# Kernel tuning notes

Hardware: AMD Instinct MI355X
Metric: run time of the kernel (lower is better)

Reference implementation:

```python
import jax, jax.numpy as jnp
import numpy as np

HIDDEN = 1152
NUM_HEADS = 16
HEAD_DIM = HIDDEN // NUM_HEADS  # 72
SEQ = 4096


def rotate_half(x):
    x1 = x[..., : x.shape[-1] // 2]
    x2 = x[..., x.shape[-1] // 2 :]
    return jnp.concatenate((-x2, x1), axis=-1)


def setup_inputs() -> dict:
    key = jax.random.key(0)
    ks = jax.random.split(key, 8)
    hidden_states = jax.random.normal(ks[0], (SEQ, HIDDEN), dtype=jnp.float32)
    cu_seqlens = jnp.sort(jax.random.randint(ks[1], (3,), 0, SEQ)).astype(jnp.int32)
    # rotary embeddings: realistic cos/sin tables
    pos = jnp.arange(SEQ, dtype=jnp.float32)[:, None]
    inv_freq = 1.0 / (10000.0 ** (jnp.arange(0, HEAD_DIM, 2, dtype=jnp.float32) / HEAD_DIM))
    freqs = pos * inv_freq[None, :]  # (SEQ, HEAD_DIM//2)
    emb = jnp.concatenate([freqs, freqs], axis=-1)  # (SEQ, HEAD_DIM)
    cos = jnp.cos(emb)
    sin = jnp.sin(emb)
    std = 0.02
    Wqkv = jax.random.normal(ks[2], (HIDDEN, 3 * HIDDEN), dtype=jnp.float32) * std
    bqkv = jnp.zeros((3 * HIDDEN,), dtype=jnp.float32)
    Wproj = jax.random.normal(ks[3], (HIDDEN, HIDDEN), dtype=jnp.float32) * std
    bproj = jnp.zeros((HIDDEN,), dtype=jnp.float32)
    return {
        "hidden_states": hidden_states,
        "cu_seqlens": cu_seqlens,
        "cos": cos,
        "sin": sin,
        "Wqkv": Wqkv,
        "bqkv": bqkv,
        "Wproj": Wproj,
        "bproj": bproj,
    }


def reference(hidden_states, cu_seqlens, cos, sin, Wqkv, bqkv, Wproj, bproj):
    seq_len = hidden_states.shape[0]
    scale = HEAD_DIM ** -0.5
    qkv = hidden_states @ Wqkv + bqkv  # (S, 3*H)
    qkv = qkv.reshape(seq_len, 3, NUM_HEADS, HEAD_DIM).transpose(1, 0, 2, 3)
    q, k, v = qkv[0], qkv[1], qkv[2]  # each (S, nH, hd)
    # inline RoPE in fp32
    orig_dtype = q.dtype
    qf = q.astype(jnp.float32)
    kf = k.astype(jnp.float32)
    c = cos[:, None, :].astype(jnp.float32)
    s = sin[:, None, :].astype(jnp.float32)
    q = (qf * c + rotate_half(qf) * s).astype(orig_dtype)
    k = (kf * c + rotate_half(kf) * s).astype(orig_dtype)
    # (nH, S, hd)
    q = q.transpose(1, 0, 2)
    k = k.transpose(1, 0, 2)
    v = v.transpose(1, 0, 2)
    attn = jnp.einsum('hqd,hkd->hqk', q, k) * scale
    attn = jax.nn.softmax(attn, axis=-1)
    out = jnp.einsum('hqk,hkd->hqd', attn, v)  # (nH, S, hd)
    out = out.transpose(1, 0, 2).reshape(seq_len, HIDDEN)
    return out @ Wproj + bproj
```

## Files before the change

### kernel.cpp

```cpp
#include <hip/hip_runtime.h>
#include <hip/hip_bf16.h>
#include <stdint.h>

#define SEQ 4096
#define HID 1152
#define NH  16
#define HD  72
#define N3  3456
#define DQ  80
#define QBLK 256
#define TILE_ELEMS 14336

typedef __bf16 bf16;
typedef __bf16 bf16x8 __attribute__((ext_vector_type(8)));
typedef float  f32x4  __attribute__((ext_vector_type(4)));
typedef float  f32x16 __attribute__((ext_vector_type(16)));
typedef uint32_t u32x4 __attribute__((ext_vector_type(4)));

#define EXP2F(x) __builtin_amdgcn_exp2f(x)
#define PLSWAP(a, b) asm("v_permlane32_swap_b32 %0, %1" : "+v"(a), "+v"(b))

__device__ __forceinline__ void gload_lds16(const void* g, void* l) {
    __builtin_amdgcn_global_load_lds(
        (__attribute__((address_space(1))) void*)(void*)g,
        (__attribute__((address_space(3))) void*)l, 16, 0, 0);
}
__device__ __forceinline__ uint16_t bfbits(float x) {
    return __builtin_bit_cast(uint16_t, (bf16)x);
}

__device__ __forceinline__ int xcd_swz(int orig, int nwg) {
    return (orig & 7) * (nwg >> 3) + (orig >> 3);
}

__global__ __launch_bounds__(256)
void prep(const float* __restrict__ hidden, const float* __restrict__ Wqkv,
          const float* __restrict__ Wproj, bf16* __restrict__ hid_b,
          bf16* __restrict__ WqkvT, bf16* __restrict__ WprojT)
{
    __shared__ float tl[32][33];
    int b = blockIdx.x, tid = threadIdx.x;
    if (b < 2304) {
        int i = b * 256 + tid;
        const float4* p = (const float4*)hidden + (size_t)i * 2;
        float4 a = p[0], c = p[1];
        bf16x8 o;
        o[0]=(bf16)a.x; o[1]=(bf16)a.y; o[2]=(bf16)a.z; o[3]=(bf16)a.w;
        o[4]=(bf16)c.x; o[5]=(bf16)c.y; o[6]=(bf16)c.z; o[7]=(bf16)c.w;
        ((bf16x8*)hid_b)[i] = o;
        return;
    }
    const float* in; bf16* out; int R, C, c0, r0;
    if (b < 6192) {
        int bb = b - 2304;
        in = Wqkv; out = WqkvT; R = HID; C = N3;
        c0 = (bb % 108) * 32; r0 = (bb / 108) * 32;
    } else {
        int bb = b - 6192;
        in = Wproj; out = WprojT; R = HID; C = HID;
        c0 = (bb % 36) * 32; r0 = (bb / 36) * 32;
    }
    int tx = tid & 31, ty = tid >> 5;
#pragma unroll
    for (int i = 0; i < 4; ++i)
        tl[ty + 8*i][tx] = in[(size_t)(r0 + ty + 8*i) * C + c0 + tx];
    __syncthreads();
#pragma unroll
    for (int i = 0; i < 4; ++i)
        out[(size_t)(c0 + ty + 8*i) * R + r0 + tx] = (bf16)tl[tx][ty + 8*i];
}

template<int OUT_F32>
__global__ __launch_bounds__(256)
void gemm_bt(const bf16* __restrict__ A, const bf16* __restrict__ BT,
             const float* __restrict__ bias, void* __restrict__ out,
             int M, int N, int K)
{
    __shared__ __align__(16) bf16 As[128 * 32];
    __shared__ __align__(16) bf16 Bs[128 * 32];
    int tid = threadIdx.x;
    int lane = tid & 63, w = tid >> 6;
    int wm = w & 1, wn = w >> 1;
    int nwg  = gridDim.x * gridDim.y;
    int wgid = xcd_swz(blockIdx.y * gridDim.x + blockIdx.x, nwg);
    int m0 = (wgid % gridDim.x) * 128, n0 = (wgid / gridDim.x) * 128;
    int lq = lane & 15, lk = lane >> 4;

    f32x4 acc[4][4] = {};

    for (int k0 = 0; k0 < K; k0 += 32) {
        __syncthreads();
#pragma unroll
        for (int i = 0; i < 2; ++i) {
            int c = w * 128 + i * 64 + lane;
            const bf16* ga = A  + (size_t)(m0 + (c >> 2)) * K + k0 + (c & 3) * 8;
            const bf16* gb = BT + (size_t)(n0 + (c >> 2)) * K + k0 + (c & 3) * 8;
            gload_lds16(ga, (char*)As + (w * 128 + i * 64) * 16);
            gload_lds16(gb, (char*)Bs + (w * 128 + i * 64) * 16);
        }
        __syncthreads();
        bf16x8 af[4], bfr[4];
#pragma unroll
        for (int m = 0; m < 4; ++m)
            af[m] = *(const bf16x8*)&As[(wm * 64 + m * 16 + lq) * 32 + lk * 8];
#pragma unroll
        for (int n = 0; n < 4; ++n)
            bfr[n] = *(const bf16x8*)&Bs[(wn * 64 + n * 16 + lq) * 32 + lk * 8];
#pragma unroll
        for (int m = 0; m < 4; ++m)
#pragma unroll
            for (int n = 0; n < 4; ++n)
                acc[m][n] = __builtin_amdgcn_mfma_f32_16x16x32_bf16(af[m], bfr[n], acc[m][n], 0, 0, 0);
    }

    int rb = m0 + wm * 64, cb = n0 + wn * 64;
#pragma unroll
    for (int m = 0; m < 4; ++m) {
#pragma unroll
        for (int n = 0; n < 4; ++n) {
            int col = cb + n * 16 + lq;
            float b = bias[col];
#pragma unroll
            for (int r = 0; r < 4; ++r) {
                int row = rb + m * 16 + lk * 4 + r;
                float v = acc[m][n][r] + b;
                if (OUT_F32) ((float*)out)[(size_t)row * N + col] = v;
                else         ((bf16*)out)[(size_t)row * N + col] = (bf16)v;
            }
        }
    }
}

__global__ __launch_bounds__(256)
void pack(const bf16* __restrict__ qkv, const float* __restrict__ cs,
          const float* __restrict__ sn, bf16* __restrict__ Qp,
          bf16* __restrict__ KVp)
{
    __shared__ __align__(16) bf16 tl[64][80];
    int b = blockIdx.x, tid = threadIdx.x;
    if (b < 32768) {
        int idx = b * 256 + tid;
        int dd = idx & 127;
        int s  = (idx >> 7) & (SEQ - 1);
        int h  = idx >> 19;
        float qv = 0.f, kv = 0.f;
        if (dd < HD) {
            const bf16* row = qkv + (size_t)s * N3 + h * HD;
            float c  = cs[s * HD + dd], si = sn[s * HD + dd];
            int   dp = (dd < 36) ? dd + 36 : dd - 36;
            float sg = (dd < 36) ? -1.f : 1.f;
            float qa = (float)row[dd],       qb = (float)row[dp];
            float ka = (float)row[HID + dd], kb = (float)row[HID + dp];
            qv = (qa * c + sg * qb * si) * (0.11785113019775793f * 1.4426950408889634f);
            kv =  ka * c + sg * kb * si;
        }
        int t = s >> 6, key = s & 63;
        int chunk = key * 16 + ((dd >> 3) ^ (key & 15));
        KVp[((size_t)(h * 64 + t)) * TILE_ELEMS + chunk * 8 + (dd & 7)] = (bf16)kv;
        if (dd < DQ) Qp[((size_t)h * SEQ + s) * DQ + dd] = (bf16)qv;
        return;
    }
    int bb = b - 32768;
    int t = bb & 63, h = bb >> 6, s0 = t * 64;
    for (int i = tid; i < 64 * 9; i += 256) {
        int key = i / 9, c8 = (i % 9) * 8;
        *(bf16x8*)&tl[key][c8] =
            *(const bf16x8*)&qkv[(size_t)(s0 + key) * N3 + 2 * HID + h * HD + c8];
    }
    __syncthreads();
    bf16* dst = KVp + ((size_t)(h * 64 + t)) * TILE_ELEMS + 8192;
    for (int vcid = tid; vcid < 768; vcid += 256) {
        int d = vcid >> 3, cpos = vcid & 7;
        int kb8 = (cpos ^ (d & 7)) << 3;
        bf16x8 v;
#pragma unroll
        for (int j = 0; j < 8; ++j)
            v[j] = (d < HD) ? tl[kb8 + j][d] : ((d == HD) ? (bf16)1.f : (bf16)0.f);
        *(bf16x8*)&dst[vcid * 8] = v;
    }
}

__global__ __launch_bounds__(512, 2)
void attn_fwd9(const bf16* __restrict__ Qp, const bf16* __restrict__ KVp,
               bf16* __restrict__ Oout)
{
    __shared__ __align__(16) char smem[114688];

    const int wgid = xcd_swz(blockIdx.x, gridDim.x);
    const int h  = wgid >> 4;
    const int q0 = (wgid & 15) * QBLK;
    const int tid = threadIdx.x, lane = tid & 63, w = tid >> 6;
    const int ql = lane & 31, hi = lane >> 5;
    const int q  = q0 + w * 32 + ql;

    bf16x8 qf[5];
    const bf16* qbase = Qp + ((size_t)h * SEQ + q) * DQ + hi * 8;
#pragma unroll
    for (int ks = 0; ks < 5; ++ks) qf[ks] = *(const bf16x8*)(qbase + ks * 16);

    int aK[5], aV[4];
#pragma unroll
    for (int ks = 0; ks < 5; ++ks)
        aK[ks] = ql * 256 + (((ks * 2 + hi) ^ (ql & 15)) * 16);
#pragma unroll
    for (int u = 0; u < 4; ++u)
        aV[u] = 16384 + ql * 128 + (((u * 2 + hi) ^ (ql & 7)) * 16);

    f32x16 o[3] = {};

    const bf16* kvbase = KVp + (size_t)h * (64 * TILE_ELEMS) + (size_t)tid * 8;

#define STAGE(T, DB) do {                                                      \
        const bf16* s_ = kvbase + (size_t)(T) * TILE_ELEMS;                    \
        char* d_ = smem + (DB) + tid * 16;                                     \
        _Pragma("unroll")                                                      \
        for (int j_ = 0; j_ < 3; ++j_)                                         \
            gload_lds16(s_ + j_ * 4096, d_ + j_ * 8192);                       \
        if (tid < 256) gload_lds16(s_ + 12288, d_ + 24576);                    \
    } while (0)

    auto compute = [&](const char* buf) {
        f32x16 sa = {}, sb = {};
        __builtin_amdgcn_s_setprio(1);
#pragma unroll
        for (int ks = 0; ks < 5; ++ks) {
            bf16x8 kf = *(const bf16x8*)(buf + aK[ks]);
            sa = __builtin_amdgcn_mfma_f32_32x32x16_bf16(kf, qf[ks], sa, 0, 0, 0);
        }
#pragma unroll
        for (int ks = 0; ks < 5; ++ks) {
            bf16x8 kf = *(const bf16x8*)(buf + 8192 + aK[ks]);
            sb = __builtin_amdgcn_mfma_f32_32x32x16_bf16(kf, qf[ks], sb, 0, 0, 0);
        }
        __builtin_amdgcn_s_setprio(0);

        uint32_t wd[16];
#pragma unroll
        for (int i = 0; i < 8; ++i) {
            wd[i]   = (uint32_t)bfbits(EXP2F(sa[2*i])) | ((uint32_t)bfbits(EXP2F(sa[2*i+1])) << 16);
            wd[8+i] = (uint32_t)bfbits(EXP2F(sb[2*i])) | ((uint32_t)bfbits(EXP2F(sb[2*i+1])) << 16);
        }

        PLSWAP(wd[0], wd[2]);   PLSWAP(wd[1], wd[3]);
        PLSWAP(wd[4], wd[6]);   PLSWAP(wd[5], wd[7]);
        PLSWAP(wd[8], wd[10]);  PLSWAP(wd[9], wd[11]);
        PLSWAP(wd[12], wd[14]); PLSWAP(wd[13], wd[15]);
        u32x4 u0 = {wd[0],wd[1],wd[2],wd[3]},   u1 = {wd[4],wd[5],wd[6],wd[7]};
        u32x4 u2 = {wd[8],wd[9],wd[10],wd[11]}, u3 = {wd[12],wd[13],wd[14],wd[15]};
        bf16x8 pb[4] = { __builtin_bit_cast(bf16x8, u0), __builtin_bit_cast(bf16x8, u1),
                         __builtin_bit_cast(bf16x8, u2), __builtin_bit_cast(bf16x8, u3) };

        __builtin_amdgcn_s_setprio(1);
#pragma unroll
        for (int db = 0; db < 3; ++db)
#pragma unroll
            for (int u = 0; u < 4; ++u) {
                bf16x8 vf = *(const bf16x8*)(buf + db * 4096 + aV[u]);
                o[db] = __builtin_amdgcn_mfma_f32_32x32x16_bf16(vf, pb[u], o[db], 0, 0, 0);
            }
        __builtin_amdgcn_s_setprio(0);
    };

#define WAIT86 do {                                                            \
        if (w < 4) asm volatile("s_waitcnt vmcnt(8)" ::: "memory");            \
        else       asm volatile("s_waitcnt vmcnt(6)" ::: "memory");            \
    } while (0)

    STAGE(0, 0); STAGE(1, 28672); STAGE(2, 57344);

    for (int tt = 0; tt < 60; tt += 4) {
#pragma unroll
        for (int j = 0; j < 4; ++j) {
            WAIT86;
            __builtin_amdgcn_s_barrier();
            STAGE(tt + j + 3, ((j + 3) & 3) * 28672);
            __builtin_amdgcn_sched_barrier(0);
            compute(smem + j * 28672);
        }
    }
    WAIT86;
    __builtin_amdgcn_s_barrier();
    STAGE(63, 86016);
    __builtin_amdgcn_sched_barrier(0);
    compute(smem);
    WAIT86;
    __builtin_amdgcn_s_barrier();
    __builtin_amdgcn_sched_barrier(0);
    compute(smem + 28672);
    if (w < 4) asm volatile("s_waitcnt vmcnt(4)" ::: "memory");
    else       asm volatile("s_waitcnt vmcnt(3)" ::: "memory");
    __builtin_amdgcn_s_barrier();
    __builtin_amdgcn_sched_barrier(0);
    compute(smem + 57344);
    asm volatile("s_waitcnt vmcnt(0)" ::: "memory");
    __builtin_amdgcn_s_barrier();
    __builtin_amdgcn_sched_barrier(0);
    compute(smem + 86016);
#undef STAGE
#undef WAIT86

    __syncthreads();
    bf16* Os = (bf16*)smem;
    {
        float lv  = o[2][4];
        float lo_ = __shfl_xor(lv, 32);
        float invl = 1.0f / (hi ? lo_ : lv);
        int qloc = w * 32 + ql;
#pragma unroll
        for (int db = 0; db < 3; ++db)
#pragma unroll
            for (int r = 0; r < 16; ++r) {
                int dloc = (r & 3) + 8 * (r >> 2) + 4 * hi;
                int d = db * 32 + dloc;
                if (d < HD) Os[qloc * 82 + d] = (bf16)(o[db][r] * invl);
            }
    }
    __syncthreads();
    for (int i = tid; i < QBLK * 36; i += 512) {
        int row = i / 36, c = i % 36;
        uint32_t val = *(const uint32_t*)((const char*)Os + row * 164 + c * 4);
        *(uint32_t*)((char*)Oout + (size_t)(q0 + row) * 2304 + h * 144 + c * 4) = val;
    }
}

extern "C" void kernel_launch(void* const* d_in, const int* in_sizes, int n_in,
                              void* d_out, int out_size, void* d_ws, size_t ws_size,
                              hipStream_t stream)
{
    const float* hidden = (const float*)d_in[0];
    const float* cosT  = (const float*)d_in[2];
    const float* sinT  = (const float*)d_in[3];
    const float* Wqkv  = (const float*)d_in[4];
    const float* bqkv  = (const float*)d_in[5];
    const float* Wproj = (const float*)d_in[6];
    const float* bproj = (const float*)d_in[7];

    char* ws = (char*)d_ws;
    size_t off = 0;
    auto alloc = [&](size_t bytes) {
        char* p = ws + off;
        off += (bytes + 255) & ~(size_t)255;
        return p;
    };
    bf16* hid_b  = (bf16*)alloc((size_t)SEQ * HID * 2);
    bf16* WqkvT  = (bf16*)alloc((size_t)N3  * HID * 2);
    bf16* WprojT = (bf16*)alloc((size_t)HID * HID * 2);
    bf16* qkv_b  = (bf16*)alloc((size_t)SEQ * N3  * 2);
    bf16* Qp     = (bf16*)alloc((size_t)NH * SEQ * DQ * 2);
    bf16* KVp    = (bf16*)alloc((size_t)NH * 64 * TILE_ELEMS * 2);
    bf16* attno  = hid_b;

    prep<<<7488, 256, 0, stream>>>(hidden, Wqkv, Wproj, hid_b, WqkvT, WprojT);
    gemm_bt<0><<<dim3(SEQ / 128, N3 / 128), 256, 0, stream>>>(hid_b, WqkvT, bqkv, qkv_b,
                                                              SEQ, N3, HID);
    pack<<<33792, 256, 0, stream>>>(qkv_b, cosT, sinT, Qp, KVp);
    attn_fwd9<<<dim3(SEQ / QBLK * NH), 512, 0, stream>>>(Qp, KVp, attno);
    gemm_bt<1><<<dim3(SEQ / 128, HID / 128), 256, 0, stream>>>(attno, WprojT, bproj, d_out,
                                                               SEQ, HID, HID);
}
```

Measured before the change: 223.9 us.

## Split KV sequence across two wave groups in 1024-thread attention blocks

The attention kernel now launches 1024 threads per block. Two groups of 8 waves each process alternate KV tiles, staged in pairs and double-buffered, and their partial outputs are summed through LDS at the end. The four-deep pipeline with fine-grained vmcnt waits is replaced by a simpler two-buffer scheme that waits on vmcnt(0) every iteration. The goal is more waves per block to hide latency, at the cost of a full drain each iteration, a reduction step, and LDS use of 120KB, which limits occupancy to one block per CU.

```diff
diff --git a/kernel.cpp b/kernel.cpp
--- a/kernel.cpp
+++ b/kernel.cpp
@@ -180,18 +180,19 @@
     }
 }
 
-__global__ __launch_bounds__(512, 2)
-void attn_fwd9(const bf16* __restrict__ Qp, const bf16* __restrict__ KVp,
-               bf16* __restrict__ Oout)
-{
-    __shared__ __align__(16) char smem[114688];
+__global__ __launch_bounds__(1024, 4)
+void attn_fwd10(const bf16* __restrict__ Qp, const bf16* __restrict__ KVp,
+                bf16* __restrict__ Oout)
+{
+    __shared__ __align__(16) char smem[122880];
 
     const int wgid = xcd_swz(blockIdx.x, gridDim.x);
     const int h  = wgid >> 4;
     const int q0 = (wgid & 15) * QBLK;
     const int tid = threadIdx.x, lane = tid & 63, w = tid >> 6;
+    const int wg = w & 7, kh = w >> 3;
     const int ql = lane & 31, hi = lane >> 5;
-    const int q  = q0 + w * 32 + ql;
+    const int q  = q0 + wg * 32 + ql;
 
     bf16x8 qf[5];
     const bf16* qbase = Qp + ((size_t)h * SEQ + q) * DQ + hi * 8;
@@ -201,35 +202,43 @@
     int aK[5], aV[4];
 #pragma unroll
     for (int ks = 0; ks < 5; ++ks)
-        aK[ks] = ql * 256 + (((ks * 2 + hi) ^ (ql & 15)) * 16);
+        aK[ks] = kh * 28672 + ql * 256 + (((ks * 2 + hi) ^ (ql & 15)) * 16);
 #pragma unroll
     for (int u = 0; u < 4; ++u)
-        aV[u] = 16384 + ql * 128 + (((u * 2 + hi) ^ (ql & 7)) * 16);
+        aV[u] = kh * 28672 + 16384 + ql * 128 + (((u * 2 + hi) ^ (ql & 7)) * 16);
 
     f32x16 o[3] = {};
 
-    const bf16* kvbase = KVp + (size_t)h * (64 * TILE_ELEMS) + (size_t)tid * 8;
-
-#define STAGE(T, DB) do {                                                      \
-        const bf16* s_ = kvbase + (size_t)(T) * TILE_ELEMS;                    \
-        char* d_ = smem + (DB) + tid * 16;                                     \
+    const bf16* kvsrc = KVp + (size_t)h * (64 * TILE_ELEMS) + (size_t)tid * 8;
+
+#define STAGE(P, BASE) do {                                                    \
+        const bf16* s_ = kvsrc + (size_t)(P) * 28672;                          \
+        char* d_ = smem + (BASE) + tid * 16;                                   \
         _Pragma("unroll")                                                      \
         for (int j_ = 0; j_ < 3; ++j_)                                         \
-            gload_lds16(s_ + j_ * 4096, d_ + j_ * 8192);                       \
-        if (tid < 256) gload_lds16(s_ + 12288, d_ + 24576);                    \
+            gload_lds16(s_ + j_ * 8192, d_ + j_ * 16384);                      \
+        if (tid < 512) gload_lds16(s_ + 24576, d_ + 49152);                    \
     } while (0)
 
-    auto compute = [&](const char* buf) {
+    STAGE(0, 0);
+    int stageBase = 65536;
+    asm volatile("s_waitcnt vmcnt(0)" ::: "memory");
+    __builtin_amdgcn_s_barrier();
+
+    for (int t = 0; t < 32; ++t) {
+        __builtin_amdgcn_sched_barrier(0);
+        if (t + 1 < 32) STAGE(t + 1, stageBase);
+
         f32x16 sa = {}, sb = {};
         __builtin_amdgcn_s_setprio(1);
 #pragma unroll
         for (int ks = 0; ks < 5; ++ks) {
-            bf16x8 kf = *(const bf16x8*)(buf + aK[ks]);
+            bf16x8 kf = *(const bf16x8*)(smem + aK[ks]);
             sa = __builtin_amdgcn_mfma_f32_32x32x16_bf16(kf, qf[ks], sa, 0, 0, 0);
         }
 #pragma unroll
         for (int ks = 0; ks < 5; ++ks) {
-            bf16x8 kf = *(const bf16x8*)(buf + 8192 + aK[ks]);
+            bf16x8 kf = *(const bf16x8*)(smem + aK[ks] + 8192);
             sb = __builtin_amdgcn_mfma_f32_32x32x16_bf16(kf, qf[ks], sb, 0, 0, 0);
         }
         __builtin_amdgcn_s_setprio(0);
@@ -255,57 +264,48 @@
         for (int db = 0; db < 3; ++db)
 #pragma unroll
             for (int u = 0; u < 4; ++u) {
-                bf16x8 vf = *(const bf16x8*)(buf + db * 4096 + aV[u]);
+                bf16x8 vf = *(const bf16x8*)(smem + aV[u] + db * 4096);
                 o[db] = __builtin_amdgcn_mfma_f32_32x32x16_bf16(vf, pb[u], o[db], 0, 0, 0);
             }
         __builtin_amdgcn_s_setprio(0);
-    };
-
-#define WAIT86 do {                                                            \
-        if (w < 4) asm volatile("s_waitcnt vmcnt(8)" ::: "memory");            \
-        else       asm volatile("s_waitcnt vmcnt(6)" ::: "memory");            \
-    } while (0)
-
-    STAGE(0, 0); STAGE(1, 28672); STAGE(2, 57344);
-
-    for (int tt = 0; tt < 60; tt += 4) {
-#pragma unroll
-        for (int j = 0; j < 4; ++j) {
-            WAIT86;
-            __builtin_amdgcn_s_barrier();
-            STAGE(tt + j + 3, ((j + 3) & 3) * 28672);
-            __builtin_amdgcn_sched_barrier(0);
-            compute(smem + j * 28672);
-        }
-    }
-    WAIT86;
-    __builtin_amdgcn_s_barrier();
-    STAGE(63, 86016);
-    __builtin_amdgcn_sched_barrier(0);
-    compute(smem);
-    WAIT86;
-    __builtin_amdgcn_s_barrier();
-    __builtin_amdgcn_sched_barrier(0);
-    compute(smem + 28672);
-    if (w < 4) asm volatile("s_waitcnt vmcnt(4)" ::: "memory");
-    else       asm volatile("s_waitcnt vmcnt(3)" ::: "memory");
-    __builtin_amdgcn_s_barrier();
-    __builtin_amdgcn_sched_barrier(0);
-    compute(smem + 57344);
-    asm volatile("s_waitcnt vmcnt(0)" ::: "memory");
-    __builtin_amdgcn_s_barrier();
-    __builtin_amdgcn_sched_barrier(0);
-    compute(smem + 86016);
+
+        __builtin_amdgcn_sched_barrier(0);
+        asm volatile("s_waitcnt vmcnt(0)" ::: "memory");
+        __builtin_amdgcn_s_barrier();
+#pragma unroll
+        for (int ks = 0; ks < 5; ++ks) aK[ks] ^= 65536;
+#pragma unroll
+        for (int u = 0; u < 4; ++u)    aV[u] ^= 65536;
+        stageBase ^= 65536;
+    }
 #undef STAGE
-#undef WAIT86
-
-    __syncthreads();
+
+    __syncthreads();
+    float* M = (float*)smem;
+    const int slot = (wg * 64 + lane) * 49;
+    if (kh == 1) {
+#pragma unroll
+        for (int db = 0; db < 3; ++db)
+#pragma unroll
+            for (int r = 0; r < 16; ++r)
+                M[slot + db * 16 + r] = o[db][r];
+    }
+    __syncthreads();
+    if (kh == 0) {
+#pragma unroll
+        for (int db = 0; db < 3; ++db)
+#pragma unroll
+            for (int r = 0; r < 16; ++r)
+                o[db][r] += M[slot + db * 16 + r];
+    }
+    __syncthreads();
+
     bf16* Os = (bf16*)smem;
-    {
+    if (kh == 0) {
         float lv  = o[2][4];
         float lo_ = __shfl_xor(lv, 32);
         float invl = 1.0f / (hi ? lo_ : lv);
-        int qloc = w * 32 + ql;
+        int qloc = wg * 32 + ql;
 #pragma unroll
         for (int db = 0; db < 3; ++db)
 #pragma unroll
@@ -316,7 +316,7 @@
             }
     }
     __syncthreads();
-    for (int i = tid; i < QBLK * 36; i += 512) {
+    for (int i = tid; i < QBLK * 36; i += 1024) {
         int row = i / 36, c = i % 36;
         uint32_t val = *(const uint32_t*)((const char*)Os + row * 164 + c * 4);
         *(uint32_t*)((char*)Oout + (size_t)(q0 + row) * 2304 + h * 144 + c * 4) = val;
@@ -354,7 +354,7 @@
     gemm_bt<0><<<dim3(SEQ / 128, N3 / 128), 256, 0, stream>>>(hid_b, WqkvT, bqkv, qkv_b,
                                                               SEQ, N3, HID);
     pack<<<33792, 256, 0, stream>>>(qkv_b, cosT, sinT, Qp, KVp);
-    attn_fwd9<<<dim3(SEQ / QBLK * NH), 512, 0, stream>>>(Qp, KVp, attno);
+    attn_fwd10<<<dim3(SEQ / QBLK * NH), 1024, 0, stream>>>(Qp, KVp, attno);
     gemm_bt<1><<<dim3(SEQ / 128, HID / 128), 256, 0, stream>>>(attno, WprojT, bproj, d_out,
                                                                SEQ, HID, HID);
 }
```

Result: no change. 221.7 us (-1.0%).

## Software-pipeline QK of next tile with softmax-PV of previous tile

Applied to the files above, without the earlier changes.

Restructures the attention main loop so the QK^T MFMAs for tile t run alongside the exp and PV MFMAs for tile t-1, using a 3-buffer LDS ring instead of a 4-deep prefetch ring. LDS drops from 114688 to 86016 bytes. The goal is to hide exp/permlane latency behind matrix work. In exchange, prefetch depth falls to one tile ahead and each step waits on vmcnt(0), which may expose global load latency. Holding the score accumulators across iterations also adds register pressure.

```diff
diff --git a/kernel.cpp b/kernel.cpp
--- a/kernel.cpp
+++ b/kernel.cpp
@@ -181,10 +181,10 @@
 }
 
 __global__ __launch_bounds__(512, 2)
-void attn_fwd9(const bf16* __restrict__ Qp, const bf16* __restrict__ KVp,
-               bf16* __restrict__ Oout)
-{
-    __shared__ __align__(16) char smem[114688];
+void attn_fwd11(const bf16* __restrict__ Qp, const bf16* __restrict__ KVp,
+                bf16* __restrict__ Oout)
+{
+    __shared__ __align__(16) char smem[86016];
 
     const int wgid = xcd_swz(blockIdx.x, gridDim.x);
     const int h  = wgid >> 4;
@@ -219,28 +219,28 @@
         if (tid < 256) gload_lds16(s_ + 12288, d_ + 24576);                    \
     } while (0)
 
-    auto compute = [&](const char* buf) {
-        f32x16 sa = {}, sb = {};
+    auto qk = [&](const char* bK, f32x16& sa, f32x16& sb) {
         __builtin_amdgcn_s_setprio(1);
 #pragma unroll
         for (int ks = 0; ks < 5; ++ks) {
-            bf16x8 kf = *(const bf16x8*)(buf + aK[ks]);
+            bf16x8 kf = *(const bf16x8*)(bK + aK[ks]);
             sa = __builtin_amdgcn_mfma_f32_32x32x16_bf16(kf, qf[ks], sa, 0, 0, 0);
         }
 #pragma unroll
         for (int ks = 0; ks < 5; ++ks) {
-            bf16x8 kf = *(const bf16x8*)(buf + 8192 + aK[ks]);
+            bf16x8 kf = *(const bf16x8*)(bK + 8192 + aK[ks]);
             sb = __builtin_amdgcn_mfma_f32_32x32x16_bf16(kf, qf[ks], sb, 0, 0, 0);
         }
         __builtin_amdgcn_s_setprio(0);
-
+    };
+
+    auto expv = [&](const f32x16& sa, const f32x16& sb, const char* bV) {
         uint32_t wd[16];
 #pragma unroll
         for (int i = 0; i < 8; ++i) {
             wd[i]   = (uint32_t)bfbits(EXP2F(sa[2*i])) | ((uint32_t)bfbits(EXP2F(sa[2*i+1])) << 16);
             wd[8+i] = (uint32_t)bfbits(EXP2F(sb[2*i])) | ((uint32_t)bfbits(EXP2F(sb[2*i+1])) << 16);
         }
-
         PLSWAP(wd[0], wd[2]);   PLSWAP(wd[1], wd[3]);
         PLSWAP(wd[4], wd[6]);   PLSWAP(wd[5], wd[7]);
         PLSWAP(wd[8], wd[10]);  PLSWAP(wd[9], wd[11]);
@@ -249,55 +249,46 @@
         u32x4 u2 = {wd[8],wd[9],wd[10],wd[11]}, u3 = {wd[12],wd[13],wd[14],wd[15]};
         bf16x8 pb[4] = { __builtin_bit_cast(bf16x8, u0), __builtin_bit_cast(bf16x8, u1),
                          __builtin_bit_cast(bf16x8, u2), __builtin_bit_cast(bf16x8, u3) };
-
         __builtin_amdgcn_s_setprio(1);
 #pragma unroll
         for (int db = 0; db < 3; ++db)
 #pragma unroll
             for (int u = 0; u < 4; ++u) {
-                bf16x8 vf = *(const bf16x8*)(buf + db * 4096 + aV[u]);
+                bf16x8 vf = *(const bf16x8*)(bV + db * 4096 + aV[u]);
                 o[db] = __builtin_amdgcn_mfma_f32_32x32x16_bf16(vf, pb[u], o[db], 0, 0, 0);
             }
         __builtin_amdgcn_s_setprio(0);
     };
 
-#define WAIT86 do {                                                            \
-        if (w < 4) asm volatile("s_waitcnt vmcnt(8)" ::: "memory");            \
-        else       asm volatile("s_waitcnt vmcnt(6)" ::: "memory");            \
-    } while (0)
-
-    STAGE(0, 0); STAGE(1, 28672); STAGE(2, 57344);
-
-    for (int tt = 0; tt < 60; tt += 4) {
-#pragma unroll
-        for (int j = 0; j < 4; ++j) {
-            WAIT86;
-            __builtin_amdgcn_s_barrier();
-            STAGE(tt + j + 3, ((j + 3) & 3) * 28672);
-            __builtin_amdgcn_sched_barrier(0);
-            compute(smem + j * 28672);
-        }
-    }
-    WAIT86;
-    __builtin_amdgcn_s_barrier();
-    STAGE(63, 86016);
-    __builtin_amdgcn_sched_barrier(0);
-    compute(smem);
-    WAIT86;
-    __builtin_amdgcn_s_barrier();
-    __builtin_amdgcn_sched_barrier(0);
-    compute(smem + 28672);
-    if (w < 4) asm volatile("s_waitcnt vmcnt(4)" ::: "memory");
-    else       asm volatile("s_waitcnt vmcnt(3)" ::: "memory");
-    __builtin_amdgcn_s_barrier();
-    __builtin_amdgcn_sched_barrier(0);
-    compute(smem + 57344);
+    f32x16 pa = {}, pb_ = {};
+
+    STAGE(0, 0);
     asm volatile("s_waitcnt vmcnt(0)" ::: "memory");
     __builtin_amdgcn_s_barrier();
-    __builtin_amdgcn_sched_barrier(0);
-    compute(smem + 86016);
+    STAGE(1, 28672);
+    qk(smem, pa, pb_);
+    asm volatile("s_waitcnt vmcnt(0)" ::: "memory");
+    __builtin_amdgcn_s_barrier();
+
+#define BODY(T, KB, VB, SB) do {                                               \
+        if ((T) < 63) STAGE((T) + 1, SB);                                      \
+        f32x16 ca = {}, cb = {};                                               \
+        qk(smem + (KB), ca, cb);                                               \
+        expv(pa, pb_, smem + (VB));                                            \
+        pa = ca; pb_ = cb;                                                     \
+        __builtin_amdgcn_sched_barrier(0);                                     \
+        asm volatile("s_waitcnt vmcnt(0)" ::: "memory");                       \
+        __builtin_amdgcn_s_barrier();                                          \
+    } while (0)
+
+    for (int t = 1; t < 64; t += 3) {
+        BODY(t,     28672, 0,     57344);
+        BODY(t + 1, 57344, 28672, 0);
+        BODY(t + 2, 0,     57344, 28672);
+    }
+    expv(pa, pb_, smem);
+#undef BODY
 #undef STAGE
-#undef WAIT86
 
     __syncthreads();
     bf16* Os = (bf16*)smem;
@@ -354,7 +345,7 @@
     gemm_bt<0><<<dim3(SEQ / 128, N3 / 128), 256, 0, stream>>>(hid_b, WqkvT, bqkv, qkv_b,
                                                               SEQ, N3, HID);
     pack<<<33792, 256, 0, stream>>>(qkv_b, cosT, sinT, Qp, KVp);
-    attn_fwd9<<<dim3(SEQ / QBLK * NH), 512, 0, stream>>>(Qp, KVp, attno);
+    attn_fwd11<<<dim3(SEQ / QBLK * NH), 512, 0, stream>>>(Qp, KVp, attno);
     gemm_bt<1><<<dim3(SEQ / 128, HID / 128), 256, 0, stream>>>(attno, WprojT, bproj, d_out,
                                                                SEQ, HID, HID);
 }
```

New measurement: 221.5 us. No clear change (-1.1%).
